# Optimization experiments

Hardware: AMD Instinct MI355X
Metric: run time of the kernel (lower is better)

The kernel has to match this reference:

```python
import jax, jax.numpy as jnp
import numpy as np

N_NODES = 100000
N_EDGES = 1600000
D_FEAT = 128
NUM_UNITS = 128


def setup_inputs() -> dict:
    key = jax.random.key(0)
    k1, k2, k3, k4, k5 = jax.random.split(key, 5)
    H = jax.random.normal(k1, (N_NODES, D_FEAT), dtype=jnp.float32)
    edge_vals = jax.random.uniform(k2, (N_EDGES,), dtype=jnp.float32)
    W = jax.random.normal(k3, (D_FEAT, NUM_UNITS), dtype=jnp.float32) / np.sqrt(D_FEAT)
    b = jnp.zeros((NUM_UNITS,), dtype=jnp.float32)
    edge_src = jax.random.randint(k4, (N_EDGES,), 0, N_NODES, dtype=jnp.int32)
    edge_dst = jax.random.randint(k5, (N_EDGES,), 0, N_NODES, dtype=jnp.int32)
    return {"H": H, "edge_vals": edge_vals, "W": W, "b": b,
            "edge_src": edge_src, "edge_dst": edge_dst}


def reference(H, edge_vals, W, b, edge_src, edge_dst):
    # SpMM: AH[i] = sum_{e: src[e]==i} val[e] * H[dst[e]]
    gathered = edge_vals[:, None] * H[edge_dst]            # [E, F]
    AH = jax.ops.segment_sum(gathered, edge_src, num_segments=N_NODES)  # [N, F]
    # Dense projection + bias + relu (tf.layers.Dense with tf.nn.relu)
    return jax.nn.relu(AH @ W + b)
```

## Files before the change

### kernel.cpp

```cpp
#include <hip/hip_runtime.h>

#define N_NODES  100000
#define N_EDGES  1600000
#define D        128
#define NBUCK    3125
#define BCAP     768
#define OCAP     8192
#define FCHUNK   4096
#define GEMM_BLOCKS 1563

typedef __attribute__((ext_vector_type(8))) short bf16x8;
typedef __attribute__((ext_vector_type(4))) float f32x4;

__device__ __forceinline__ unsigned short f2bf(float x) {
    unsigned u = __float_as_uint(x);
    u += 0x7fffu + ((u >> 16) & 1u);
    return (unsigned short)(u >> 16);
}

__global__ __launch_bounds__(256) void mega(
    const float* __restrict__ H, const float* __restrict__ W,
    const int* __restrict__ src, const int* __restrict__ dst,
    const float* __restrict__ vals, unsigned short* __restrict__ HWb,
    int* __restrict__ ccursor, int2* __restrict__ sedge_raw,
    int4* __restrict__ oflow, int* __restrict__ oflow_cnt)
{
    __shared__ char smem[32768];
    const int t = threadIdx.x;

    if (blockIdx.x < GEMM_BLOCKS) {
        short* wlds = (short*)smem;
        {
            const int n   = t & 127;
            const int kb0 = (t >> 7) * 4;
            const int c = n >> 4, cc = n & 15;
#pragma unroll
            for (int q = 0; q < 16; ++q) {
                int kbase = q * 8 + kb0;
                float w0 = W[(kbase + 0) * 128 + n];
                float w1 = W[(kbase + 1) * 128 + n];
                float w2 = W[(kbase + 2) * 128 + n];
                float w3 = W[(kbase + 3) * 128 + n];
                int ks = kbase >> 5, g = (kbase >> 3) & 3, j0 = kbase & 7;
                short4 pk;
                pk.x = (short)f2bf(w0);
                pk.y = (short)f2bf(w1);
                pk.z = (short)f2bf(w2);
                pk.w = (short)f2bf(w3);
                *reinterpret_cast<short4*>(
                    &wlds[(size_t)(((c * 4 + ks) * 64) + g * 16 + cc) * 8 + j0]) = pk;
            }
        }
        __syncthreads();

        const int wid  = t >> 6;
        const int lane = t & 63;
        const int row16 = blockIdx.x * 64 + wid * 16;
        const int g = lane >> 4;

        int arow = row16 + (lane & 15);
        if (arow >= N_NODES) arow = N_NODES - 1;

        f32x4 acc[8];
#pragma unroll
        for (int c = 0; c < 8; ++c) acc[c] = (f32x4){0.f, 0.f, 0.f, 0.f};

#pragma unroll
        for (int ks = 0; ks < 4; ++ks) {
            const float* ap = H + (size_t)arow * D + ks * 32 + g * 8;
            float4 a0 = *reinterpret_cast<const float4*>(ap);
            float4 a1 = *reinterpret_cast<const float4*>(ap + 4);
            bf16x8 af;
            af[0] = (short)f2bf(a0.x); af[1] = (short)f2bf(a0.y);
            af[2] = (short)f2bf(a0.z); af[3] = (short)f2bf(a0.w);
            af[4] = (short)f2bf(a1.x); af[5] = (short)f2bf(a1.y);
            af[6] = (short)f2bf(a1.z); af[7] = (short)f2bf(a1.w);
#pragma unroll
            for (int c = 0; c < 8; ++c) {
                bf16x8 bf = *reinterpret_cast<const bf16x8*>(
                    &wlds[(size_t)((c * 4 + ks) * 64 + lane) * 8]);
                acc[c] = __builtin_amdgcn_mfma_f32_16x16x32_bf16(af, bf, acc[c], 0, 0, 0);
            }
        }

#pragma unroll
        for (int c = 0; c < 8; ++c) {
#pragma unroll
            for (int r = 0; r < 4; ++r) {
                int orow = row16 + g * 4 + r;
                if (orow < N_NODES)
                    HWb[(size_t)orow * D + c * 16 + (lane & 15)] = f2bf(acc[c][r]);
            }
        }
    } else {
        int* lhist = (int*)smem;
        int* lbase = lhist + NBUCK;
        for (int i = t; i < NBUCK; i += 256) lhist[i] = 0;
        __syncthreads();
        const int fb = blockIdx.x - GEMM_BLOCKS;
        const int e0 = fb * FCHUNK;
        const int e1 = min(e0 + FCHUNK, N_EDGES);
        for (int e = e0 + t; e < e1; e += 256)
            atomicAdd(&lhist[src[e] >> 5], 1);
        __syncthreads();
        for (int i = t; i < NBUCK; i += 256) {
            int c = lhist[i];
            lbase[i] = c ? atomicAdd(&ccursor[i], c) : 0;
            lhist[i] = 0;
        }
        __syncthreads();
        for (int e = e0 + t; e < e1; e += 256) {
            int s = src[e];
            int bkt = s >> 5;
            int pos = lbase[bkt] + atomicAdd(&lhist[bkt], 1);
            if (pos < BCAP) {
                int2 p;
                p.x = dst[e] | ((s & 31) << 17);
                p.y = __float_as_int(vals[e]);
                sedge_raw[(size_t)bkt * BCAP + pos] = p;
            } else {
                int oc = atomicAdd(oflow_cnt, 1);
                if (oc < OCAP) oflow[oc] = make_int4(s, dst[e], __float_as_int(vals[e]), 0);
            }
        }
    }
}

__global__ __launch_bounds__(256) void sort_gather(
    const unsigned short* __restrict__ HWb, const int2* __restrict__ sedge_raw,
    const int* __restrict__ ccursor, const int4* __restrict__ oflow,
    const int* __restrict__ oflow_cnt, const float* __restrict__ bias,
    float* __restrict__ out)
{
    __shared__ int2 eLds[BCAP];
    __shared__ int h[32];
    __shared__ int ex[32];
    __shared__ int cur[32];
    const int bkt = blockIdx.x;
    const int t = threadIdx.x;
    const size_t base = (size_t)bkt * BCAP;
    const int cnt = min(ccursor[bkt], BCAP);

    if (t < 32) { h[t] = 0; }
    __syncthreads();

    int2 myE[3]; int myR[3];
#pragma unroll
    for (int q = 0; q < 3; ++q) {
        int j = t + q * 256;
        myR[q] = -1;
        if (j < cnt) {
            myE[q] = sedge_raw[base + j];
            myR[q] = (myE[q].x >> 17) & 31;
            atomicAdd(&h[myR[q]], 1);
        }
    }
    __syncthreads();
    if (t < 32) {
        int v = h[t];
        int x = v;
        for (int off = 1; off < 32; off <<= 1) {
            int y = __shfl_up(x, off);
            if (t >= off) x += y;
        }
        ex[t] = x - v;
        cur[t] = 0;
    }
    __syncthreads();
#pragma unroll
    for (int q = 0; q < 3; ++q) {
        if (myR[q] >= 0) {
            int pos = ex[myR[q]] + atomicAdd(&cur[myR[q]], 1);
            int2 e;
            e.x = myE[q].x & 0x1FFFF;
            e.y = myE[q].y;
            eLds[pos] = e;
        }
    }
    __syncthreads();

    const int wid = t >> 6, lane = t & 63;
    const int ovc = *oflow_cnt;
    const float2 bv = *reinterpret_cast<const float2*>(bias + lane * 2);
    for (int ln = wid; ln < 32; ln += 4) {
        int node = bkt * 32 + ln;
        const int j0 = ex[ln], j1 = ex[ln] + h[ln];
        float ax = 0.f, ay = 0.f, bx = 0.f, by = 0.f;
        float cx = 0.f, cy = 0.f, dx = 0.f, dy = 0.f;
        int j = j0;
        for (; j + 4 <= j1; j += 4) {
            int2 e0 = eLds[j],     e1 = eLds[j + 1];
            int2 e2 = eLds[j + 2], e3 = eLds[j + 3];
            unsigned u0 = *reinterpret_cast<const unsigned*>(HWb + (size_t)e0.x * D + lane * 2);
            unsigned u1 = *reinterpret_cast<const unsigned*>(HWb + (size_t)e1.x * D + lane * 2);
            unsigned u2 = *reinterpret_cast<const unsigned*>(HWb + (size_t)e2.x * D + lane * 2);
            unsigned u3 = *reinterpret_cast<const unsigned*>(HWb + (size_t)e3.x * D + lane * 2);
            float v0 = __int_as_float(e0.y), v1 = __int_as_float(e1.y);
            float v2 = __int_as_float(e2.y), v3 = __int_as_float(e3.y);
            ax += v0 * __uint_as_float(u0 << 16);
            ay += v0 * __uint_as_float(u0 & 0xffff0000u);
            bx += v1 * __uint_as_float(u1 << 16);
            by += v1 * __uint_as_float(u1 & 0xffff0000u);
            cx += v2 * __uint_as_float(u2 << 16);
            cy += v2 * __uint_as_float(u2 & 0xffff0000u);
            dx += v3 * __uint_as_float(u3 << 16);
            dy += v3 * __uint_as_float(u3 & 0xffff0000u);
        }
        for (; j < j1; ++j) {
            int2 e = eLds[j];
            unsigned u = *reinterpret_cast<const unsigned*>(HWb + (size_t)e.x * D + lane * 2);
            float v = __int_as_float(e.y);
            ax += v * __uint_as_float(u << 16);
            ay += v * __uint_as_float(u & 0xffff0000u);
        }
        for (int q = 0; q < ovc; ++q) {
            int4 e = oflow[q];
            if (e.x == node) {
                unsigned u = *reinterpret_cast<const unsigned*>(HWb + (size_t)e.y * D + lane * 2);
                float v = __int_as_float(e.z);
                ax += v * __uint_as_float(u << 16);
                ay += v * __uint_as_float(u & 0xffff0000u);
            }
        }
        float2 o;
        o.x = fmaxf((ax + bx) + (cx + dx) + bv.x, 0.f);
        o.y = fmaxf((ay + by) + (cy + dy) + bv.y, 0.f);
        *reinterpret_cast<float2*>(out + (size_t)node * D + lane * 2) = o;
    }
}

extern "C" void kernel_launch(void* const* d_in, const int* in_sizes, int n_in,
                              void* d_out, int out_size, void* d_ws, size_t ws_size,
                              hipStream_t stream) {
    const float* H    = (const float*)d_in[0];
    const float* vals = (const float*)d_in[1];
    const float* W    = (const float*)d_in[2];
    const float* b    = (const float*)d_in[3];
    const int*   src  = (const int*)d_in[4];
    const int*   dst  = (const int*)d_in[5];
    float* out = (float*)d_out;

    unsigned short* HWb = (unsigned short*)d_ws;
    int2* sedge_raw = (int2*)(HWb + (size_t)N_NODES * D);
    int*  ccursor   = (int*)(sedge_raw + (size_t)NBUCK * BCAP);
    int*  oflow_cnt = ccursor + NBUCK;
    int4* oflow     = (int4*)(oflow_cnt + 3);

    hipMemsetAsync(ccursor, 0, (NBUCK + 1) * sizeof(int), stream);

    const int FILL_BLOCKS = (N_EDGES + FCHUNK - 1) / FCHUNK;
    mega<<<GEMM_BLOCKS + FILL_BLOCKS, 256, 0, stream>>>(
        H, W, src, dst, vals, HWb, ccursor, sedge_raw, oflow, oflow_cnt);
    sort_gather<<<NBUCK, 256, 0, stream>>>(HWb, sedge_raw, ccursor, oflow,
                                           oflow_cnt, b, out);
}
```

Before: 128.1 us.

## Precompute bf16 W fragments once, pack LDS histogram, schedule fill blocks first

A small init kernel now zeroes the bucket cursors (replacing the memset) and converts W once into a bf16 fragment layout in global memory. GEMM blocks then read B fragments straight from global/L2 instead of each block rebuilding W in LDS. The edge bucketing histogram packs two 16-bit counters per word, halving LDS use, and fill blocks now come first in the grid so the atomic-heavy work starts early. The trade is an extra launch and B operands fetched from cache rather than LDS.

```diff
diff --git a/kernel.cpp b/kernel.cpp
--- a/kernel.cpp
+++ b/kernel.cpp
@@ -7,7 +7,9 @@
 #define BCAP     768
 #define OCAP     8192
 #define FCHUNK   4096
+#define FILL_BLOCKS ((N_EDGES + FCHUNK - 1) / FCHUNK)
 #define GEMM_BLOCKS 1563
+#define NPACK    ((NBUCK + 1) / 2)
 
 typedef __attribute__((ext_vector_type(8))) short bf16x8;
 typedef __attribute__((ext_vector_type(4))) float f32x4;
@@ -18,44 +20,70 @@
     return (unsigned short)(u >> 16);
 }
 
-__global__ __launch_bounds__(256) void mega(
-    const float* __restrict__ H, const float* __restrict__ W,
+__global__ __launch_bounds__(256) void init_kernel(
+    const float* __restrict__ W, unsigned short* __restrict__ Wfrag,
+    int* __restrict__ ccursor)
+{
+    int t = blockIdx.x * 256 + threadIdx.x;
+    if (t <= NBUCK) ccursor[t] = 0;
+    int k = t >> 7, n = t & 127;
+    int c = n >> 4, cc = n & 15, ks = k >> 5, g = (k >> 3) & 3, j = k & 7;
+    int lane = g * 16 + cc;
+    Wfrag[(size_t)(((c * 4 + ks) * 64) + lane) * 8 + j] = f2bf(W[t]);
+}
+
+__global__ __launch_bounds__(256) void mega2(
+    const float* __restrict__ H, const unsigned short* __restrict__ Wfrag,
     const int* __restrict__ src, const int* __restrict__ dst,
     const float* __restrict__ vals, unsigned short* __restrict__ HWb,
     int* __restrict__ ccursor, int2* __restrict__ sedge_raw,
     int4* __restrict__ oflow, int* __restrict__ oflow_cnt)
 {
-    __shared__ char smem[32768];
+    __shared__ unsigned lhistP[NPACK];
+    __shared__ unsigned lbaseP[NPACK];
     const int t = threadIdx.x;
 
-    if (blockIdx.x < GEMM_BLOCKS) {
-        short* wlds = (short*)smem;
-        {
-            const int n   = t & 127;
-            const int kb0 = (t >> 7) * 4;
-            const int c = n >> 4, cc = n & 15;
-#pragma unroll
-            for (int q = 0; q < 16; ++q) {
-                int kbase = q * 8 + kb0;
-                float w0 = W[(kbase + 0) * 128 + n];
-                float w1 = W[(kbase + 1) * 128 + n];
-                float w2 = W[(kbase + 2) * 128 + n];
-                float w3 = W[(kbase + 3) * 128 + n];
-                int ks = kbase >> 5, g = (kbase >> 3) & 3, j0 = kbase & 7;
-                short4 pk;
-                pk.x = (short)f2bf(w0);
-                pk.y = (short)f2bf(w1);
-                pk.z = (short)f2bf(w2);
-                pk.w = (short)f2bf(w3);
-                *reinterpret_cast<short4*>(
-                    &wlds[(size_t)(((c * 4 + ks) * 64) + g * 16 + cc) * 8 + j0]) = pk;
-            }
-        }
+    if (blockIdx.x < FILL_BLOCKS) {
+        for (int i = t; i < NPACK; i += 256) lhistP[i] = 0;
         __syncthreads();
-
+        const int e0 = blockIdx.x * FCHUNK;
+        const int e1 = min(e0 + FCHUNK, N_EDGES);
+        for (int e = e0 + t; e < e1; e += 256) {
+            int b = src[e] >> 5;
+            atomicAdd(&lhistP[b >> 1], 1u << ((b & 1) << 4));
+        }
+        __syncthreads();
+        for (int i = t; i < NPACK; i += 256) {
+            unsigned p = lhistP[i];
+            unsigned c0 = p & 0xffffu, c1 = p >> 16;
+            unsigned b0 = c0 ? (unsigned)atomicAdd(&ccursor[2 * i], (int)c0) : 0u;
+            unsigned b1 = c1 ? (unsigned)atomicAdd(&ccursor[2 * i + 1], (int)c1) : 0u;
+            lbaseP[i] = (b0 & 0xffffu) | (b1 << 16);
+            lhistP[i] = 0;
+        }
+        __syncthreads();
+        for (int e = e0 + t; e < e1; e += 256) {
+            int s = src[e];
+            int b = s >> 5;
+            unsigned sh = (unsigned)(b & 1) << 4;
+            unsigned old = atomicAdd(&lhistP[b >> 1], 1u << sh);
+            int pos = (int)((lbaseP[b >> 1] >> sh) & 0xffffu) +
+                      (int)((old >> sh) & 0xffffu);
+            if (pos < BCAP) {
+                int2 p;
+                p.x = dst[e] | ((s & 31) << 17);
+                p.y = __float_as_int(vals[e]);
+                sedge_raw[(size_t)b * BCAP + pos] = p;
+            } else {
+                int oc = atomicAdd(oflow_cnt, 1);
+                if (oc < OCAP) oflow[oc] = make_int4(s, dst[e], __float_as_int(vals[e]), 0);
+            }
+        }
+    } else {
+        const int gb   = blockIdx.x - FILL_BLOCKS;
         const int wid  = t >> 6;
         const int lane = t & 63;
-        const int row16 = blockIdx.x * 64 + wid * 16;
+        const int row16 = gb * 64 + wid * 16;
         const int g = lane >> 4;
 
         int arow = row16 + (lane & 15);
@@ -78,7 +106,7 @@
 #pragma unroll
             for (int c = 0; c < 8; ++c) {
                 bf16x8 bf = *reinterpret_cast<const bf16x8*>(
-                    &wlds[(size_t)((c * 4 + ks) * 64 + lane) * 8]);
+                    Wfrag + (size_t)((c * 4 + ks) * 64 + lane) * 8);
                 acc[c] = __builtin_amdgcn_mfma_f32_16x16x32_bf16(af, bf, acc[c], 0, 0, 0);
             }
         }
@@ -90,37 +118,6 @@
                 int orow = row16 + g * 4 + r;
                 if (orow < N_NODES)
                     HWb[(size_t)orow * D + c * 16 + (lane & 15)] = f2bf(acc[c][r]);
-            }
-        }
-    } else {
-        int* lhist = (int*)smem;
-        int* lbase = lhist + NBUCK;
-        for (int i = t; i < NBUCK; i += 256) lhist[i] = 0;
-        __syncthreads();
-        const int fb = blockIdx.x - GEMM_BLOCKS;
-        const int e0 = fb * FCHUNK;
-        const int e1 = min(e0 + FCHUNK, N_EDGES);
-        for (int e = e0 + t; e < e1; e += 256)
-            atomicAdd(&lhist[src[e] >> 5], 1);
-        __syncthreads();
-        for (int i = t; i < NBUCK; i += 256) {
-            int c = lhist[i];
-            lbase[i] = c ? atomicAdd(&ccursor[i], c) : 0;
-            lhist[i] = 0;
-        }
-        __syncthreads();
-        for (int e = e0 + t; e < e1; e += 256) {
-            int s = src[e];
-            int bkt = s >> 5;
-            int pos = lbase[bkt] + atomicAdd(&lhist[bkt], 1);
-            if (pos < BCAP) {
-                int2 p;
-                p.x = dst[e] | ((s & 31) << 17);
-                p.y = __float_as_int(vals[e]);
-                sedge_raw[(size_t)bkt * BCAP + pos] = p;
-            } else {
-                int oc = atomicAdd(oflow_cnt, 1);
-                if (oc < OCAP) oflow[oc] = make_int4(s, dst[e], __float_as_int(vals[e]), 0);
             }
         }
     }
@@ -240,17 +237,16 @@
     const int*   dst  = (const int*)d_in[5];
     float* out = (float*)d_out;
 
-    unsigned short* HWb = (unsigned short*)d_ws;
-    int2* sedge_raw = (int2*)(HWb + (size_t)N_NODES * D);
+    unsigned short* HWb   = (unsigned short*)d_ws;
+    unsigned short* Wfrag = HWb + (size_t)N_NODES * D;
+    int2* sedge_raw = (int2*)(Wfrag + 128 * 128);
     int*  ccursor   = (int*)(sedge_raw + (size_t)NBUCK * BCAP);
     int*  oflow_cnt = ccursor + NBUCK;
     int4* oflow     = (int4*)(oflow_cnt + 3);
 
-    hipMemsetAsync(ccursor, 0, (NBUCK + 1) * sizeof(int), stream);
-
-    const int FILL_BLOCKS = (N_EDGES + FCHUNK - 1) / FCHUNK;
-    mega<<<GEMM_BLOCKS + FILL_BLOCKS, 256, 0, stream>>>(
-        H, W, src, dst, vals, HWb, ccursor, sedge_raw, oflow, oflow_cnt);
+    init_kernel<<<64, 256, 0, stream>>>(W, Wfrag, ccursor);
+    mega2<<<FILL_BLOCKS + GEMM_BLOCKS, 256, 0, stream>>>(
+        H, Wfrag, src, dst, vals, HWb, ccursor, sedge_raw, oflow, oflow_cnt);
     sort_gather<<<NBUCK, 256, 0, stream>>>(HWb, sedge_raw, ccursor, oflow,
                                            oflow_cnt, b, out);
 }
```

Result: no change. 129.0 us (+0.7%).
